# Performance work log

Measured on AMD Instinct MI355X. Metric: run time of the kernel, lower is better.

The kernel has to match this reference:

```python
import jax, jax.numpy as jnp
import numpy as np

N_NODES = 100000
N_EDGES = 1600000
N_GRAPHS = 512
IN_C, HID_C, OUT_C = 128, 128, 64


def setup_inputs() -> dict:
    key = jax.random.key(0)
    ks = jax.random.split(key, 10)
    x = jax.random.normal(ks[0], (N_NODES, IN_C), dtype=jnp.float32)
    edge_index = jax.random.randint(ks[1], (2, N_EDGES), 0, N_NODES, dtype=jnp.int64)
    batch = jnp.sort(jax.random.randint(ks[2], (N_NODES,), 0, N_GRAPHS, dtype=jnp.int64))
    def glorot(k, shape):
        fan_in = shape[1]
        return jax.random.normal(k, shape, dtype=jnp.float32) / jnp.sqrt(jnp.float32(fan_in))
    return {
        "x": x, "edge_index": edge_index, "batch": batch,
        "w_nbr0": glorot(ks[3], (HID_C, IN_C)), "w_self0": glorot(ks[4], (HID_C, IN_C)), "b0": jnp.zeros((HID_C,), jnp.float32),
        "w_nbr1": glorot(ks[5], (HID_C, HID_C)), "w_self1": glorot(ks[6], (HID_C, HID_C)), "b1": jnp.zeros((HID_C,), jnp.float32),
        "w_nbr2": glorot(ks[7], (OUT_C, HID_C)), "w_self2": glorot(ks[8], (OUT_C, HID_C)), "b2": jnp.zeros((OUT_C,), jnp.float32),
    }


def _sage_conv(x, src, dst, w_nbr, w_self, b):
    n = x.shape[0]
    # mean aggregation of neighbor messages: gather x[src], segment-sum at dst
    agg = jax.ops.segment_sum(x[src], dst, num_segments=n)  # [N, d]
    deg = jax.ops.segment_sum(jnp.ones_like(dst, dtype=x.dtype), dst, num_segments=n)
    mean_nbr = agg / jnp.maximum(deg, 1.0)[:, None]
    return mean_nbr @ w_nbr.T + x @ w_self.T + b


def reference(x, edge_index, batch, w_nbr0, w_self0, b0, w_nbr1, w_self1, b1, w_nbr2, w_self2, b2):
    src, dst = edge_index[0], edge_index[1]
    h = jax.nn.relu(_sage_conv(x, src, dst, w_nbr0, w_self0, b0))
    h = jax.nn.relu(_sage_conv(h, src, dst, w_nbr1, w_self1, b1))
    h = _sage_conv(h, src, dst, w_nbr2, w_self2, b2)
    # global mean pool over graphs in the batch
    sums = jax.ops.segment_sum(h, batch, num_segments=N_GRAPHS)  # [G, out]
    cnts = jax.ops.segment_sum(jnp.ones_like(batch, dtype=h.dtype), batch, num_segments=N_GRAPHS)
    return sums / jnp.maximum(cnts, 1.0)[:, None]
```

## Files before the change

kernel.cpp:

```cpp
#include <hip/hip_runtime.h>
#include <hip/hip_bf16.h>

#define NGRAPHS 512
#define BCAP 8192

typedef __attribute__((ext_vector_type(8))) short bf16x8;
typedef __attribute__((ext_vector_type(4))) float f32x4;

__device__ inline short f2bf(float x) {
    __hip_bfloat16 h = __float2bfloat16(x);
    return *(short*)&h;
}


__global__ __launch_bounds__(256) void k_bscatter(const int* __restrict__ src,
                                                  const int* __restrict__ dst,
                                                  int* __restrict__ bcur,
                                                  uint* __restrict__ pairs,
                                                  int nE, int NB) {
    __shared__ int cnt[512];
    __shared__ int gbase[512];
    const int t = threadIdx.x;
    const int seg0 = blockIdx.x * 4096;

    for (int l = t; l < NB; l += 256) cnt[l] = 0;
    __syncthreads();

    int sv[16], bv[16], rv[16];
#pragma unroll
    for (int k = 0; k < 16; ++k) {
        int e = seg0 + k * 256 + t;
        if (e < nE) {
            int d = dst[e];
            bv[k] = d >> 8;
            rv[k] = atomicAdd(&cnt[bv[k]], 1);
            sv[k] = src[e] | ((d & 255) << 20);
        } else {
            bv[k] = -1;
        }
    }
    __syncthreads();
    for (int l = t; l < NB; l += 256) {
        int c = cnt[l];
        gbase[l] = (c > 0) ? atomicAdd(&bcur[l], c) : 0;
    }
    __syncthreads();
#pragma unroll
    for (int k = 0; k < 16; ++k) {
        if (bv[k] >= 0) {
            int pos = gbase[bv[k]] + rv[k];
            if (pos < BCAP) pairs[(size_t)bv[k] * BCAP + pos] = (uint)sv[k];
        }
    }
}

__global__ __launch_bounds__(256) void k_bbuild(const int* __restrict__ bcur,
                                                const uint* __restrict__ pairs,
                                                int* __restrict__ row_start,
                                                int* __restrict__ row_end,
                                                float* __restrict__ rdeg,
                                                int* __restrict__ col, int n) {
    __shared__ int s[256];
    __shared__ int cur[256];
    const int b = blockIdx.x;
    const int t = threadIdx.x;
    const uint* bp = pairs + (size_t)b * BCAP;
    int cnt = bcur[b];
    if (cnt > BCAP) cnt = BCAP;

    s[t] = 0;
    __syncthreads();
    for (int i = t; i < cnt; i += 256) {
        int local = bp[i] >> 20;
        atomicAdd(&s[local], 1);
    }
    __syncthreads();
    int my = s[t];
    for (int off = 1; off < 256; off <<= 1) {
        int v = (t >= off) ? s[t - off] : 0;
        __syncthreads();
        s[t] += v;
        __syncthreads();
    }
    int excl = s[t] - my;
    int v = b * 256 + t;
    if (v < n) {
        row_start[v] = b * BCAP + excl;
        row_end[v] = b * BCAP + excl + my;
        rdeg[v] = 1.0f / (float)(my > 1 ? my : 1);
    }
    cur[t] = excl;
    __syncthreads();
    for (int i = t; i < cnt; i += 256) {
        uint u = bp[i];
        int local = u >> 20;
        int pos = atomicAdd(&cur[local], 1);
        col[(size_t)b * BCAP + pos] = (int)(u & 0xFFFFFu);
    }
}


__global__ __launch_bounds__(256) void k_cast(const float* __restrict__ x,
                                              ushort* __restrict__ xb, int total4) {
    int i = blockIdx.x * 256 + threadIdx.x;
    if (i >= total4) return;
    float4 v = ((const float4*)x)[i];
    ushort4 o;
    o.x = (ushort)f2bf(v.x);
    o.y = (ushort)f2bf(v.y);
    o.z = (ushort)f2bf(v.z);
    o.w = (ushort)f2bf(v.w);
    ((ushort4*)xb)[i] = o;
}


__global__ __launch_bounds__(256) void k_agg(const ushort* __restrict__ h,
                                             const int* __restrict__ row_start,
                                             const int* __restrict__ row_end,
                                             const int* __restrict__ col,
                                             const float* __restrict__ rdeg,
                                             ushort* __restrict__ out, int n) {
    int w = (blockIdx.x * blockDim.x + threadIdx.x) >> 6;
    int lane = threadIdx.x & 63;
    if (w >= n) return;
    int s = row_start[w], e = row_end[w];
    int grp = lane >> 4;
    int cl = lane & 15;

    float a0 = 0.f, a1 = 0.f, a2 = 0.f, a3 = 0.f, a4 = 0.f, a5 = 0.f, a6 = 0.f, a7 = 0.f;

    if (e > s) {
        int cfirst = col[s];
        for (int j = s; j < e; j += 8) {
            int j0 = j + grp, j1 = j + 4 + grp;
            bool ok0 = j0 < e, ok1 = j1 < e;
            int c0 = ok0 ? col[j0] : cfirst;
            int c1 = ok1 ? col[j1] : cfirst;
            uint4 r0 = *(const uint4*)(h + (size_t)c0 * 128 + cl * 8);
            uint4 r1 = *(const uint4*)(h + (size_t)c1 * 128 + cl * 8);
            if (ok0) {
                a0 += __uint_as_float(r0.x << 16); a1 += __uint_as_float(r0.x & 0xffff0000u);
                a2 += __uint_as_float(r0.y << 16); a3 += __uint_as_float(r0.y & 0xffff0000u);
                a4 += __uint_as_float(r0.z << 16); a5 += __uint_as_float(r0.z & 0xffff0000u);
                a6 += __uint_as_float(r0.w << 16); a7 += __uint_as_float(r0.w & 0xffff0000u);
            }
            if (ok1) {
                a0 += __uint_as_float(r1.x << 16); a1 += __uint_as_float(r1.x & 0xffff0000u);
                a2 += __uint_as_float(r1.y << 16); a3 += __uint_as_float(r1.y & 0xffff0000u);
                a4 += __uint_as_float(r1.z << 16); a5 += __uint_as_float(r1.z & 0xffff0000u);
                a6 += __uint_as_float(r1.w << 16); a7 += __uint_as_float(r1.w & 0xffff0000u);
            }
        }
        a0 += __shfl_xor(a0, 16); a1 += __shfl_xor(a1, 16);
        a2 += __shfl_xor(a2, 16); a3 += __shfl_xor(a3, 16);
        a4 += __shfl_xor(a4, 16); a5 += __shfl_xor(a5, 16);
        a6 += __shfl_xor(a6, 16); a7 += __shfl_xor(a7, 16);
        a0 += __shfl_xor(a0, 32); a1 += __shfl_xor(a1, 32);
        a2 += __shfl_xor(a2, 32); a3 += __shfl_xor(a3, 32);
        a4 += __shfl_xor(a4, 32); a5 += __shfl_xor(a5, 32);
        a6 += __shfl_xor(a6, 32); a7 += __shfl_xor(a7, 32);
    }

    if (grp == 0) {
        float r = rdeg[w];
        uint4 o;
        o.x = (uint)(ushort)f2bf(a0 * r) | ((uint)(ushort)f2bf(a1 * r) << 16);
        o.y = (uint)(ushort)f2bf(a2 * r) | ((uint)(ushort)f2bf(a3 * r) << 16);
        o.z = (uint)(ushort)f2bf(a4 * r) | ((uint)(ushort)f2bf(a5 * r) << 16);
        o.w = (uint)(ushort)f2bf(a6 * r) | ((uint)(ushort)f2bf(a7 * r) << 16);
        *(uint4*)(out + (size_t)w * 128 + cl * 8) = o;
    }
}


__global__ void k_wprep(const float* __restrict__ wn, const float* __restrict__ ws,
                        short* __restrict__ whi, short* __restrict__ wlo, int outc) {
    int i = blockIdx.x * 256 + threadIdx.x;
    if (i >= outc * 256) return;
    int c = i >> 8, k = i & 255;
    float w = (k < 128) ? wn[c * 128 + k] : ws[c * 128 + k - 128];
    short hi = f2bf(w);
    __hip_bfloat16 hb = *(__hip_bfloat16*)&hi;
    float hif = __bfloat162float(hb);
    whi[i] = hi;
    wlo[i] = f2bf(w - hif);
}


template <int OUTC, bool RELU, int CHUNK>
__global__ __launch_bounds__(256, 2) void k_transform_mfma(
    const ushort* __restrict__ meanbuf, const ushort* __restrict__ hbuf,
    const bf16x8* __restrict__ whi, const bf16x8* __restrict__ wlo,
    const float* __restrict__ bias, ushort* __restrict__ out, int n) {
    constexpr int NCF = OUTC / 64;
    const int wave = threadIdx.x >> 6;
    const int lane = threadIdx.x & 63;
    const int lmod = lane & 15, lgrp = lane >> 4;
    const int n0 = wave * (NCF * 16);

    bf16x8 bh[NCF][8], bl[NCF][8];
#pragma unroll
    for (int cf = 0; cf < NCF; ++cf) {
        int c = n0 + cf * 16 + lmod;
#pragma unroll
        for (int ks = 0; ks < 8; ++ks) {
            int idx = c * 32 + ks * 4 + lgrp;
            bh[cf][ks] = whi[idx];
            bl[cf][ks] = wlo[idx];
        }
    }

    const int tile0 = blockIdx.x * CHUNK;
    for (int t = 0; t < CHUNK; ++t) {
        int row0 = (tile0 + t) * 16;
        if (row0 >= n) break;
        int m = row0 + lmod;
        const ushort* mrow = meanbuf + (size_t)m * 128;
        const ushort* hrow = hbuf + (size_t)m * 128;

        bf16x8 af[8];
#pragma unroll
        for (int ks = 0; ks < 4; ++ks) af[ks] = *(const bf16x8*)(mrow + ks * 32 + lgrp * 8);
#pragma unroll
        for (int ks = 0; ks < 4; ++ks) af[4 + ks] = *(const bf16x8*)(hrow + ks * 32 + lgrp * 8);

        f32x4 acc[NCF];
#pragma unroll
        for (int cf = 0; cf < NCF; ++cf) acc[cf] = (f32x4){0.f, 0.f, 0.f, 0.f};
#pragma unroll
        for (int ks = 0; ks < 8; ++ks) {
#pragma unroll
            for (int cf = 0; cf < NCF; ++cf) {
                acc[cf] = __builtin_amdgcn_mfma_f32_16x16x32_bf16(af[ks], bh[cf][ks], acc[cf], 0, 0, 0);
                acc[cf] = __builtin_amdgcn_mfma_f32_16x16x32_bf16(af[ks], bl[cf][ks], acc[cf], 0, 0, 0);
            }
        }

#pragma unroll
        for (int cf = 0; cf < NCF; ++cf) {
            int c = n0 + cf * 16 + lmod;
            float bv = bias[c];
#pragma unroll
            for (int r = 0; r < 4; ++r) {
                int rr = row0 + lgrp * 4 + r;
                float v = acc[cf][r] + bv;
                if (RELU) v = fmaxf(v, 0.f);
                out[(size_t)rr * OUTC + c] = (ushort)f2bf(v);
            }
        }
    }
}


__global__ void k_gbounds(const int* __restrict__ batch, int* __restrict__ gstart, int n) {
    int g = blockIdx.x * blockDim.x + threadIdx.x;
    if (g > NGRAPHS) return;
    int lo = 0, hi = n;
    while (lo < hi) {
        int mid = (lo + hi) >> 1;
        if (batch[mid] < g) lo = mid + 1; else hi = mid;
    }
    gstart[g] = lo;
}

__global__ __launch_bounds__(256) void k_pool2(const ushort* __restrict__ h,
                                               const int* __restrict__ gstart,
                                               float* __restrict__ out) {
    int g = blockIdx.x;
    int t = threadIdx.x, lane = t & 63, wv = t >> 6;
    int s = gstart[g], e = gstart[g + 1];
    float acc = 0.f;
    for (int i = s + wv; i < e; i += 4) {
        uint v = h[(size_t)i * 64 + lane];
        acc += __uint_as_float(v << 16);
    }
    __shared__ float red[4][64];
    red[wv][lane] = acc;
    __syncthreads();
    if (wv == 0) {
        float tot = red[0][lane] + red[1][lane] + red[2][lane] + red[3][lane];
        float c = (float)(e - s);
        out[g * 64 + lane] = tot / fmaxf(c, 1.0f);
    }
}


extern "C" void kernel_launch(void* const* d_in, const int* in_sizes, int n_in,
                              void* d_out, int out_size, void* d_ws, size_t ws_size,
                              hipStream_t stream) {
    const float* x = (const float*)d_in[0];
    const int* ei = (const int*)d_in[1];
    const int* batch = (const int*)d_in[2];
    const float* wn0 = (const float*)d_in[3];
    const float* ws0 = (const float*)d_in[4];
    const float* b0 = (const float*)d_in[5];
    const float* wn1 = (const float*)d_in[6];
    const float* ws1 = (const float*)d_in[7];
    const float* b1 = (const float*)d_in[8];
    const float* wn2 = (const float*)d_in[9];
    const float* ws2 = (const float*)d_in[10];
    const float* b2 = (const float*)d_in[11];

    const int n = in_sizes[0] / 128;
    const int nE = in_sizes[1] / 2;
    const int* src = ei;
    const int* dst = ei + nE;
    const int NB = (n + 255) >> 8;

    char* p = (char*)d_ws;
    auto alloc = [&](size_t bytes) {
        void* r = (void*)p;
        p += (bytes + 255) & ~(size_t)255;
        return r;
    };
    int* bcur = (int*)alloc((size_t)NB * 4);
    uint* pairs = (uint*)alloc((size_t)NB * BCAP * 4);
    int* col = (int*)alloc((size_t)NB * BCAP * 4);
    int* row_start = (int*)alloc((size_t)NB * 256 * 4);
    int* row_end = (int*)alloc((size_t)NB * 256 * 4);
    float* rdeg = (float*)alloc((size_t)NB * 256 * 4);
    int* gstart = (int*)alloc((size_t)(NGRAPHS + 1) * 4);
    short* whi0 = (short*)alloc(128 * 256 * 2);
    short* wlo0 = (short*)alloc(128 * 256 * 2);
    short* whi1 = (short*)alloc(128 * 256 * 2);
    short* wlo1 = (short*)alloc(128 * 256 * 2);
    short* whi2 = (short*)alloc(64 * 256 * 2);
    short* wlo2 = (short*)alloc(64 * 256 * 2);
    ushort* xb = (ushort*)alloc((size_t)n * 128 * 2);
    ushort* meanb = (ushort*)alloc((size_t)n * 128 * 2);
    ushort* h1 = (ushort*)alloc((size_t)n * 128 * 2);
    ushort* h2 = (ushort*)alloc((size_t)n * 128 * 2);
    ushort* h3 = (ushort*)alloc((size_t)n * 64 * 2);

    (void)hipMemsetAsync(bcur, 0, (size_t)NB * 4, stream);

    const int tb = 256;

    k_bscatter<<<(nE + 4095) / 4096, tb, 0, stream>>>(src, dst, bcur, pairs, nE, NB);
    k_bbuild<<<NB, tb, 0, stream>>>(bcur, pairs, row_start, row_end, rdeg, col, n);

    k_cast<<<((n * 128 / 4) + 255) / 256, 256, 0, stream>>>(x, xb, n * 128 / 4);

    k_wprep<<<(128 * 256 + 255) / 256, 256, 0, stream>>>(wn0, ws0, whi0, wlo0, 128);
    k_wprep<<<(128 * 256 + 255) / 256, 256, 0, stream>>>(wn1, ws1, whi1, wlo1, 128);
    k_wprep<<<(64 * 256 + 255) / 256, 256, 0, stream>>>(wn2, ws2, whi2, wlo2, 64);

    k_gbounds<<<3, 256, 0, stream>>>(batch, gstart, n);

    const int aggGrid = ((n * 64) + tb - 1) / tb;
    const int nTiles = (n + 15) / 16;
    const int CH = 13;
    const int tGrid = (nTiles + CH - 1) / CH;

    k_agg<<<aggGrid, tb, 0, stream>>>(xb, row_start, row_end, col, rdeg, meanb, n);
    k_transform_mfma<128, true, 13><<<tGrid, 256, 0, stream>>>(
        meanb, xb, (const bf16x8*)whi0, (const bf16x8*)wlo0, b0, h1, n);
    k_agg<<<aggGrid, tb, 0, stream>>>(h1, row_start, row_end, col, rdeg, meanb, n);
    k_transform_mfma<128, true, 13><<<tGrid, 256, 0, stream>>>(
        meanb, h1, (const bf16x8*)whi1, (const bf16x8*)wlo1, b1, h2, n);
    k_agg<<<aggGrid, tb, 0, stream>>>(h2, row_start, row_end, col, rdeg, meanb, n);
    k_transform_mfma<64, false, 13><<<tGrid, 256, 0, stream>>>(
        meanb, h2, (const bf16x8*)whi2, (const bf16x8*)wlo2, b2, h3, n);

    k_pool2<<<NGRAPHS, 256, 0, stream>>>(h3, gstart, (float*)d_out);
}
```

Before: 375.8 us.

## Transform-then-aggregate in last layer and restage transform tiles through swizzled LDS

The last SAGE layer now applies both weight matrices first, producing 64 neighbor-projected and 64 self-projected columns per node. It then aggregates only the 64-wide neighbor part and adds the self part, so the costly gather moves 64 channels instead of 128. The MFMA transform is rewritten to stage input tiles through double-buffered, XOR-swizzled shared memory, with 512 threads per block, one 16-column slab per wave and separate hi/lo accumulators. This adds extra bf16 rounding of the intermediate before aggregation and changes the grid and occupancy of the transform.

Result: faster. 359.5 us (-4.3%).

```diff
diff --git a/kernel.cpp b/kernel.cpp
--- a/kernel.cpp
+++ b/kernel.cpp
@@ -11,6 +11,8 @@
     __hip_bfloat16 h = __float2bfloat16(x);
     return *(short*)&h;
 }
+__device__ inline float bflo(uint v) { return __uint_as_float(v << 16); }
+__device__ inline float bfhi(uint v) { return __uint_as_float(v & 0xffff0000u); }
 
 
 __global__ __launch_bounds__(256) void k_bscatter(const int* __restrict__ src,
@@ -139,16 +141,16 @@
             uint4 r0 = *(const uint4*)(h + (size_t)c0 * 128 + cl * 8);
             uint4 r1 = *(const uint4*)(h + (size_t)c1 * 128 + cl * 8);
             if (ok0) {
-                a0 += __uint_as_float(r0.x << 16); a1 += __uint_as_float(r0.x & 0xffff0000u);
-                a2 += __uint_as_float(r0.y << 16); a3 += __uint_as_float(r0.y & 0xffff0000u);
-                a4 += __uint_as_float(r0.z << 16); a5 += __uint_as_float(r0.z & 0xffff0000u);
-                a6 += __uint_as_float(r0.w << 16); a7 += __uint_as_float(r0.w & 0xffff0000u);
+                a0 += bflo(r0.x); a1 += bfhi(r0.x);
+                a2 += bflo(r0.y); a3 += bfhi(r0.y);
+                a4 += bflo(r0.z); a5 += bfhi(r0.z);
+                a6 += bflo(r0.w); a7 += bfhi(r0.w);
             }
             if (ok1) {
-                a0 += __uint_as_float(r1.x << 16); a1 += __uint_as_float(r1.x & 0xffff0000u);
-                a2 += __uint_as_float(r1.y << 16); a3 += __uint_as_float(r1.y & 0xffff0000u);
-                a4 += __uint_as_float(r1.z << 16); a5 += __uint_as_float(r1.z & 0xffff0000u);
-                a6 += __uint_as_float(r1.w << 16); a7 += __uint_as_float(r1.w & 0xffff0000u);
+                a0 += bflo(r1.x); a1 += bfhi(r1.x);
+                a2 += bflo(r1.y); a3 += bfhi(r1.y);
+                a4 += bflo(r1.z); a5 += bfhi(r1.z);
+                a6 += bflo(r1.w); a7 += bfhi(r1.w);
             }
         }
         a0 += __shfl_xor(a0, 16); a1 += __shfl_xor(a1, 16);
@@ -172,6 +174,57 @@
     }
 }
 
+
+__global__ __launch_bounds__(256) void k_agg2(const ushort* __restrict__ t2,
+                                              const int* __restrict__ row_start,
+                                              const int* __restrict__ row_end,
+                                              const int* __restrict__ col,
+                                              const float* __restrict__ rdeg,
+                                              ushort* __restrict__ out, int n) {
+    int w = (blockIdx.x * blockDim.x + threadIdx.x) >> 6;
+    int lane = threadIdx.x & 63;
+    if (w >= n) return;
+    int s = row_start[w], e = row_end[w];
+    int grp = lane >> 4;
+    int cl = lane & 15;
+
+    float a0 = 0.f, a1 = 0.f, a2 = 0.f, a3 = 0.f;
+
+    if (e > s) {
+        int cfirst = col[s];
+        for (int j = s; j < e; j += 8) {
+            int j0 = j + grp, j1 = j + 4 + grp;
+            bool ok0 = j0 < e, ok1 = j1 < e;
+            int c0 = ok0 ? col[j0] : cfirst;
+            int c1 = ok1 ? col[j1] : cfirst;
+            uint2 r0 = *(const uint2*)(t2 + (size_t)c0 * 128 + cl * 4);
+            uint2 r1 = *(const uint2*)(t2 + (size_t)c1 * 128 + cl * 4);
+            if (ok0) {
+                a0 += bflo(r0.x); a1 += bfhi(r0.x);
+                a2 += bflo(r0.y); a3 += bfhi(r0.y);
+            }
+            if (ok1) {
+                a0 += bflo(r1.x); a1 += bfhi(r1.x);
+                a2 += bflo(r1.y); a3 += bfhi(r1.y);
+            }
+        }
+        a0 += __shfl_xor(a0, 16); a1 += __shfl_xor(a1, 16);
+        a2 += __shfl_xor(a2, 16); a3 += __shfl_xor(a3, 16);
+        a0 += __shfl_xor(a0, 32); a1 += __shfl_xor(a1, 32);
+        a2 += __shfl_xor(a2, 32); a3 += __shfl_xor(a3, 32);
+    }
+
+    if (grp == 0) {
+        float r = rdeg[w];
+        uint2 tsv = *(const uint2*)(t2 + (size_t)w * 128 + 64 + cl * 4);
+        float t0 = bflo(tsv.x), t1 = bfhi(tsv.x);
+        float t2v = bflo(tsv.y), t3 = bfhi(tsv.y);
+        uint2 o;
+        o.x = (uint)(ushort)f2bf(a0 * r + t0) | ((uint)(ushort)f2bf(a1 * r + t1) << 16);
+        o.y = (uint)(ushort)f2bf(a2 * r + t2v) | ((uint)(ushort)f2bf(a3 * r + t3) << 16);
+        *(uint2*)(out + (size_t)w * 64 + cl * 4) = o;
+    }
+}
 
 __global__ void k_wprep(const float* __restrict__ wn, const float* __restrict__ ws,
                         short* __restrict__ whi, short* __restrict__ wlo, int outc) {
@@ -186,67 +239,115 @@
     wlo[i] = f2bf(w - hif);
 }
 
-
-template <int OUTC, bool RELU, int CHUNK>
-__global__ __launch_bounds__(256, 2) void k_transform_mfma(
+__global__ void k_wprep2(const float* __restrict__ wn, const float* __restrict__ ws,
+                         short* __restrict__ whi, short* __restrict__ wlo) {
+    int i = blockIdx.x * 256 + threadIdx.x;
+    if (i >= 128 * 128) return;
+    int c = i >> 7, k = i & 127;
+    float w = (c < 64) ? wn[c * 128 + k] : ws[(c - 64) * 128 + k];
+    short hi = f2bf(w);
+    __hip_bfloat16 hb = *(__hip_bfloat16*)&hi;
+    float hif = __bfloat162float(hb);
+    whi[i] = hi;
+    wlo[i] = f2bf(w - hif);
+}
+
+
+template <int KH, bool RELU, bool HALFBIAS, int CHUNK>
+__global__ __launch_bounds__(512) void k_transform2(
     const ushort* __restrict__ meanbuf, const ushort* __restrict__ hbuf,
     const bf16x8* __restrict__ whi, const bf16x8* __restrict__ wlo,
-    const float* __restrict__ bias, ushort* __restrict__ out, int n) {
-    constexpr int NCF = OUTC / 64;
-    const int wave = threadIdx.x >> 6;
-    const int lane = threadIdx.x & 63;
+    const float* __restrict__ bias, ushort* __restrict__ out, int n, int nTiles) {
+    constexpr int ROWB = KH * 256;
+    constexpr int KS = KH * 4;
+    __shared__ ushort lds[2][16 * KH * 128];
+
+    const int t = threadIdx.x;
+    const int wave = t >> 6, lane = t & 63;
     const int lmod = lane & 15, lgrp = lane >> 4;
-    const int n0 = wave * (NCF * 16);
-
-    bf16x8 bh[NCF][8], bl[NCF][8];
-#pragma unroll
-    for (int cf = 0; cf < NCF; ++cf) {
-        int c = n0 + cf * 16 + lmod;
-#pragma unroll
-        for (int ks = 0; ks < 8; ++ks) {
-            int idx = c * 32 + ks * 4 + lgrp;
-            bh[cf][ks] = whi[idx];
-            bl[cf][ks] = wlo[idx];
-        }
-    }
-
+    const int c = wave * 16 + lmod;
+
+    bf16x8 bh[KS], bl[KS];
+#pragma unroll
+    for (int ks = 0; ks < KS; ++ks) {
+        int idx = c * (KH * 16) + ks * 4 + lgrp;
+        bh[ks] = whi[idx];
+        bl[ks] = wlo[idx];
+    }
+    float bv;
+    if (HALFBIAS) bv = (c >= 64) ? bias[c - 64] : 0.f;
+    else bv = bias[c];
+
+    const int srow = t >> 5;
+    const int seg = t & 31;
     const int tile0 = blockIdx.x * CHUNK;
-    for (int t = 0; t < CHUNK; ++t) {
-        int row0 = (tile0 + t) * 16;
-        if (row0 >= n) break;
-        int m = row0 + lmod;
-        const ushort* mrow = meanbuf + (size_t)m * 128;
-        const ushort* hrow = hbuf + (size_t)m * 128;
-
-        bf16x8 af[8];
-#pragma unroll
-        for (int ks = 0; ks < 4; ++ks) af[ks] = *(const bf16x8*)(mrow + ks * 32 + lgrp * 8);
-#pragma unroll
-        for (int ks = 0; ks < 4; ++ks) af[4 + ks] = *(const bf16x8*)(hrow + ks * 32 + lgrp * 8);
-
-        f32x4 acc[NCF];
-#pragma unroll
-        for (int cf = 0; cf < NCF; ++cf) acc[cf] = (f32x4){0.f, 0.f, 0.f, 0.f};
-#pragma unroll
-        for (int ks = 0; ks < 8; ++ks) {
-#pragma unroll
-            for (int cf = 0; cf < NCF; ++cf) {
-                acc[cf] = __builtin_amdgcn_mfma_f32_16x16x32_bf16(af[ks], bh[cf][ks], acc[cf], 0, 0, 0);
-                acc[cf] = __builtin_amdgcn_mfma_f32_16x16x32_bf16(af[ks], bl[cf][ks], acc[cf], 0, 0, 0);
+    if (tile0 >= nTiles) return;
+    const int nt = (nTiles - tile0 < CHUNK) ? (nTiles - tile0) : CHUNK;
+    const int swr = (srow * ROWB + seg * (KH == 2 ? 16 : 8)) ^ ((srow & 7) << 4);
+
+    uint4 R;
+    {
+        int m = tile0 * 16 + srow; if (m >= n) m = n - 1;
+        if constexpr (KH == 2) {
+            const ushort* sp = (seg < 16) ? (meanbuf + (size_t)m * 128 + seg * 8)
+                                          : (hbuf + (size_t)m * 128 + (seg - 16) * 8);
+            R = *(const uint4*)sp;
+        } else {
+            uint2 r2 = *(const uint2*)(hbuf + (size_t)m * 128 + seg * 4);
+            R.x = r2.x; R.y = r2.y;
+        }
+    }
+    if constexpr (KH == 2) *(uint4*)((char*)lds[0] + swr) = R;
+    else { uint2 r2; r2.x = R.x; r2.y = R.y; *(uint2*)((char*)lds[0] + swr) = r2; }
+    {
+        int m = (tile0 + 1) * 16 + srow; if (m >= n) m = n - 1;
+        if constexpr (KH == 2) {
+            const ushort* sp = (seg < 16) ? (meanbuf + (size_t)m * 128 + seg * 8)
+                                          : (hbuf + (size_t)m * 128 + (seg - 16) * 8);
+            R = *(const uint4*)sp;
+        } else {
+            uint2 r2 = *(const uint2*)(hbuf + (size_t)m * 128 + seg * 4);
+            R.x = r2.x; R.y = r2.y;
+        }
+    }
+
+    for (int tt = 0; tt < nt; ++tt) {
+        __syncthreads();
+        if (tt + 1 < nt) {
+            if constexpr (KH == 2) *(uint4*)((char*)lds[(tt + 1) & 1] + swr) = R;
+            else { uint2 r2; r2.x = R.x; r2.y = R.y; *(uint2*)((char*)lds[(tt + 1) & 1] + swr) = r2; }
+        }
+        if (tt + 2 < nt) {
+            int m = (tile0 + tt + 2) * 16 + srow; if (m >= n) m = n - 1;
+            if constexpr (KH == 2) {
+                const ushort* sp = (seg < 16) ? (meanbuf + (size_t)m * 128 + seg * 8)
+                                              : (hbuf + (size_t)m * 128 + (seg - 16) * 8);
+                R = *(const uint4*)sp;
+            } else {
+                uint2 r2 = *(const uint2*)(hbuf + (size_t)m * 128 + seg * 4);
+                R.x = r2.x; R.y = r2.y;
             }
         }
 
-#pragma unroll
-        for (int cf = 0; cf < NCF; ++cf) {
-            int c = n0 + cf * 16 + lmod;
-            float bv = bias[c];
-#pragma unroll
-            for (int r = 0; r < 4; ++r) {
-                int rr = row0 + lgrp * 4 + r;
-                float v = acc[cf][r] + bv;
-                if (RELU) v = fmaxf(v, 0.f);
-                out[(size_t)rr * OUTC + c] = (ushort)f2bf(v);
-            }
+        bf16x8 af[KS];
+#pragma unroll
+        for (int ks = 0; ks < KS; ++ks) {
+            int byte = (lmod * ROWB + ks * 64 + lgrp * 16) ^ ((lmod & 7) << 4);
+            af[ks] = *(const bf16x8*)((const char*)lds[tt & 1] + byte);
+        }
+        f32x4 ah = {0.f, 0.f, 0.f, 0.f}, al = {0.f, 0.f, 0.f, 0.f};
+#pragma unroll
+        for (int ks = 0; ks < KS; ++ks) {
+            ah = __builtin_amdgcn_mfma_f32_16x16x32_bf16(af[ks], bh[ks], ah, 0, 0, 0);
+            al = __builtin_amdgcn_mfma_f32_16x16x32_bf16(af[ks], bl[ks], al, 0, 0, 0);
+        }
+        int row0 = (tile0 + tt) * 16;
+#pragma unroll
+        for (int r = 0; r < 4; ++r) {
+            int rr = row0 + lgrp * 4 + r;
+            float v = ah[r] + al[r] + bv;
+            if (RELU) v = fmaxf(v, 0.f);
+            if (rr < n) out[(size_t)rr * 128 + c] = (ushort)f2bf(v);
         }
     }
 }
@@ -324,8 +425,8 @@
     short* wlo0 = (short*)alloc(128 * 256 * 2);
     short* whi1 = (short*)alloc(128 * 256 * 2);
     short* wlo1 = (short*)alloc(128 * 256 * 2);
-    short* whi2 = (short*)alloc(64 * 256 * 2);
-    short* wlo2 = (short*)alloc(64 * 256 * 2);
+    short* whi2 = (short*)alloc(128 * 128 * 2);
+    short* wlo2 = (short*)alloc(128 * 128 * 2);
     ushort* xb = (ushort*)alloc((size_t)n * 128 * 2);
     ushort* meanb = (ushort*)alloc((size_t)n * 128 * 2);
     ushort* h1 = (ushort*)alloc((size_t)n * 128 * 2);
@@ -343,24 +444,23 @@
 
     k_wprep<<<(128 * 256 + 255) / 256, 256, 0, stream>>>(wn0, ws0, whi0, wlo0, 128);
     k_wprep<<<(128 * 256 + 255) / 256, 256, 0, stream>>>(wn1, ws1, whi1, wlo1, 128);
-    k_wprep<<<(64 * 256 + 255) / 256, 256, 0, stream>>>(wn2, ws2, whi2, wlo2, 64);
+    k_wprep2<<<(128 * 128 + 255) / 256, 256, 0, stream>>>(wn2, ws2, whi2, wlo2);
 
     k_gbounds<<<3, 256, 0, stream>>>(batch, gstart, n);
 
     const int aggGrid = ((n * 64) + tb - 1) / tb;
     const int nTiles = (n + 15) / 16;
-    const int CH = 13;
-    const int tGrid = (nTiles + CH - 1) / CH;
+    const int tGrid = (nTiles + 3) / 4;
 
     k_agg<<<aggGrid, tb, 0, stream>>>(xb, row_start, row_end, col, rdeg, meanb, n);
-    k_transform_mfma<128, true, 13><<<tGrid, 256, 0, stream>>>(
-        meanb, xb, (const bf16x8*)whi0, (const bf16x8*)wlo0, b0, h1, n);
+    k_transform2<2, true, false, 4><<<tGrid, 512, 0, stream>>>(
+        meanb, xb, (const bf16x8*)whi0, (const bf16x8*)wlo0, b0, h1, n, nTiles);
     k_agg<<<aggGrid, tb, 0, stream>>>(h1, row_start, row_end, col, rdeg, meanb, n);
-    k_transform_mfma<128, true, 13><<<tGrid, 256, 0, stream>>>(
-        meanb, h1, (const bf16x8*)whi1, (const bf16x8*)wlo1, b1, h2, n);
-    k_agg<<<aggGrid, tb, 0, stream>>>(h2, row_start, row_end, col, rdeg, meanb, n);
-    k_transform_mfma<64, false, 13><<<tGrid, 256, 0, stream>>>(
-        meanb, h2, (const bf16x8*)whi2, (const bf16x8*)wlo2, b2, h3, n);
+    k_transform2<2, true, false, 4><<<tGrid, 512, 0, stream>>>(
+        meanb, h1, (const bf16x8*)whi1, (const bf16x8*)wlo1, b1, h2, n, nTiles);
+    k_transform2<1, false, true, 4><<<tGrid, 512, 0, stream>>>(
+        h2, h2, (const bf16x8*)whi2, (const bf16x8*)wlo2, b2, meanb, n, nTiles);
+    k_agg2<<<aggGrid, tb, 0, stream>>>(meanb, row_start, row_end, col, rdeg, h3, n);
 
     k_pool2<<<NGRAPHS, 256, 0, stream>>>(h3, gstart, (float*)d_out);
 }
```
